# Kernel optimization log

Hardware: AMD Instinct MI355X
Metric: run time of the kernel (lower is better)

The kernel has to match this reference:

```python
import jax, jax.numpy as jnp
import numpy as np

DIM = 768
NUM_HEADS = 12
HEAD_DIM = DIM // NUM_HEADS
ALL_HEAD_DIM = HEAD_DIM * NUM_HEADS
SCALE = HEAD_DIM ** -0.5


def setup_inputs() -> dict:
    key = jax.random.key(0)
    k1, k2, k3, k4 = jax.random.split(key, 4)
    B, N = 8, 1024
    x = jax.random.normal(k1, (B, N, DIM), dtype=jnp.float32)
    # qkv_bias=False -> no qkv bias; proj has bias (nn.Linear default)
    w_qkv = jax.random.normal(k2, (DIM, 3 * ALL_HEAD_DIM), dtype=jnp.float32) * (DIM ** -0.5)
    w_proj = jax.random.normal(k3, (ALL_HEAD_DIM, DIM), dtype=jnp.float32) * (ALL_HEAD_DIM ** -0.5)
    b_proj = jax.random.normal(k4, (DIM,), dtype=jnp.float32) * 0.02
    return {"x": x, "w_qkv": w_qkv, "w_proj": w_proj, "b_proj": b_proj}


def reference(x, w_qkv, w_proj, b_proj):
    B, N, C = x.shape
    qkv = (x @ w_qkv).reshape(B, N, 3, NUM_HEADS, HEAD_DIM)
    qkv = jnp.transpose(qkv, (2, 0, 3, 1, 4))  # [3, B, H, N, D]
    q, k, v = qkv[0], qkv[1], qkv[2]
    attn = jax.nn.softmax(jnp.einsum('bhnd,bhmd->bhnm', q * SCALE, k), axis=-1)
    out = jnp.einsum('bhnm,bhmd->bhnd', attn, v)  # [B, H, N, D]
    out = jnp.transpose(out, (0, 2, 1, 3)).reshape(B, N, ALL_HEAD_DIM)
    return out @ w_proj + b_proj
```

## Files before the change

### kernel.cpp

```cpp
#include <hip/hip_runtime.h>
#include <hip/hip_bf16.h>

#define NH 12
#define HD 64
#define SEQ 1024
#define BATCH 8
#define DIM 768
#define QKVN 2304
#define ROWS 8192

typedef __bf16 bf16x8 __attribute__((ext_vector_type(8)));
typedef float f32x4 __attribute__((ext_vector_type(4)));
typedef unsigned short u16x8 __attribute__((ext_vector_type(8)));
typedef unsigned short u16x4 __attribute__((ext_vector_type(4)));
typedef short s16x4 __attribute__((ext_vector_type(4)));

__device__ __forceinline__ unsigned short f2bf(float f) {
  union { float f; unsigned int u; } c; c.f = f;
  unsigned int u = c.u;
  u += 0x7fffu + ((u >> 16) & 1u);
  return (unsigned short)(u >> 16);
}

__device__ __forceinline__ unsigned int pk_bf16(float a, float b) {
  union { __hip_bfloat162 h; unsigned int w; } u;
  u.h = __float22bfloat162_rn(float2{a, b});
  return u.w;
}

__device__ __forceinline__ void gload_lds16(const unsigned short* g, unsigned short* l) {
  __builtin_amdgcn_global_load_lds(
      (const __attribute__((address_space(1))) void*)g,
      (__attribute__((address_space(3))) void*)l, 16, 0, 0);
}

__device__ __forceinline__ void tr_tile(const float* __restrict__ src, unsigned short* __restrict__ dst,
                                        int R, int C, int bx, int by, float tile[32][33]) {
  int tx = threadIdx.x & 31, ty = threadIdx.x >> 5;
  int c0 = bx * 32, r0 = by * 32;
#pragma unroll
  for (int i = 0; i < 4; ++i)
    tile[ty + i * 8][tx] = src[(size_t)(r0 + ty + i * 8) * C + c0 + tx];
  __syncthreads();
#pragma unroll
  for (int i = 0; i < 4; ++i)
    dst[(size_t)(c0 + ty + i * 8) * R + r0 + tx] = f2bf(tile[tx][ty + i * 8]);
}

__global__ void prep_kernel(const float* __restrict__ x, unsigned short* __restrict__ xb,
                            const float* __restrict__ w_qkv, unsigned short* __restrict__ wqkvT,
                            const float* __restrict__ w_proj, unsigned short* __restrict__ wprojT) {
  __shared__ float tile[32][33];
  int blk = blockIdx.x;
  if (blk < 6144) {
    int i = blk * 256 + threadIdx.x;
    float4 v = ((const float4*)x)[i];
    unsigned int lo = pk_bf16(v.x, v.y), hi = pk_bf16(v.z, v.w);
    union { unsigned int w[2]; u16x4 o; } u; u.w[0] = lo; u.w[1] = hi;
    ((u16x4*)xb)[i] = u.o;
  } else if (blk < 6144 + 1728) {
    int t = blk - 6144;
    tr_tile(w_qkv, wqkvT, DIM, QKVN, t % 72, t / 72, tile);
  } else {
    int t = blk - 6144 - 1728;
    tr_tile(w_proj, wprojT, DIM, DIM, t % 24, t / 24, tile);
  }
}

template <bool BF16_OUT, bool SCALE_Q>
__global__ __launch_bounds__(256, 3) void gemm192(
    const unsigned short* __restrict__ A, const unsigned short* __restrict__ BT,
    void* __restrict__ Cout, const float* __restrict__ bias,
    int M, int N, int K, int nbyXCD) {
  __shared__ unsigned short As[2][128 * 32];
  __shared__ unsigned short Bs[2][192 * 32];
  const int tid = threadIdx.x;
  const int wave = tid >> 6, lane = tid & 63, quad = lane >> 4, l16 = lane & 15;
  const int wm = wave >> 1, wn = wave & 1;
  const int g = blockIdx.x & 7, bi = blockIdx.x >> 3;
  const int by = g * nbyXCD + (bi % nbyXCD);
  const int bx = bi / nbyXCD;
  const int bm = by * 128, bn = bx * 192;

  const int r0 = tid >> 2, kc0 = (tid & 3) * 8;
  const unsigned short* Ag = A + (size_t)(bm + r0) * K + kc0;
  const unsigned short* Bg = BT + (size_t)(bn + r0) * K + kc0;
  unsigned short* AsB = &As[0][0];
  unsigned short* BsB = &Bs[0][0];
  const int wdst = (tid & ~63) * 8;

#define STAGE_G(kt, b) do {                                                   \
    int koff_ = (kt) * 32;                                                    \
    gload_lds16(Ag + koff_,                    AsB + (b) * 4096 + wdst);      \
    gload_lds16(Ag + koff_ + (size_t)64 * K,   AsB + (b) * 4096 + wdst + 2048);\
    gload_lds16(Bg + koff_,                    BsB + (b) * 6144 + wdst);      \
    gload_lds16(Bg + koff_ + (size_t)64 * K,   BsB + (b) * 6144 + wdst + 2048);\
    gload_lds16(Bg + koff_ + (size_t)128 * K,  BsB + (b) * 6144 + wdst + 4096);\
  } while (0)

  f32x4 zero4 = {0.f, 0.f, 0.f, 0.f};
  f32x4 acc[4][6];
#pragma unroll
  for (int i = 0; i < 4; ++i)
#pragma unroll
    for (int j = 0; j < 6; ++j) acc[i][j] = zero4;

  const int nkt = K >> 5;
  STAGE_G(0, 0);
  for (int kt = 0; kt < nkt; ++kt) {
    __syncthreads();
    if (kt + 1 < nkt) STAGE_G(kt + 1, (kt + 1) & 1);
    const unsigned short* Ab = AsB + (kt & 1) * 4096;
    const unsigned short* Bb = BsB + (kt & 1) * 6144;
    bf16x8 af[4], bf[6];
#pragma unroll
    for (int mt = 0; mt < 4; ++mt)
      af[mt] = *(const bf16x8*)&Ab[(wm * 64 + mt * 16 + l16) * 32 + quad * 8];
#pragma unroll
    for (int nt = 0; nt < 6; ++nt)
      bf[nt] = *(const bf16x8*)&Bb[(wn * 96 + nt * 16 + l16) * 32 + quad * 8];
#pragma unroll
    for (int mt = 0; mt < 4; ++mt)
#pragma unroll
      for (int nt = 0; nt < 6; ++nt)
        acc[mt][nt] = __builtin_amdgcn_mfma_f32_16x16x32_bf16(af[mt], bf[nt], acc[mt][nt], 0, 0, 0);
  }
#undef STAGE_G

#pragma unroll
  for (int mt = 0; mt < 4; ++mt)
#pragma unroll
    for (int nt = 0; nt < 6; ++nt) {
      int col = bn + wn * 96 + nt * 16 + l16;
      float bv = BF16_OUT ? 0.f : bias[col];
      float scl = (SCALE_Q && col < DIM) ? 0.125f : 1.0f;
#pragma unroll
      for (int r = 0; r < 4; ++r) {
        int row = bm + wm * 64 + mt * 16 + quad * 4 + r;
        float v = acc[mt][nt][r];
        if (BF16_OUT)
          ((unsigned short*)Cout)[(size_t)row * N + col] = f2bf(v * scl);
        else
          ((float*)Cout)[(size_t)row * N + col] = v + bv;
      }
    }
}

__global__ __launch_bounds__(256, 5) void gemm64_proj(
    const unsigned short* __restrict__ A, const unsigned short* __restrict__ BT,
    float* __restrict__ Cout, const float* __restrict__ bias,
    int M, int N, int K, int nbyXCD) {
  __shared__ unsigned short As[2][128 * 32];
  __shared__ unsigned short Bs[2][64 * 32];
  const int tid = threadIdx.x;
  const int wave = tid >> 6, lane = tid & 63, quad = lane >> 4, l16 = lane & 15;
  const int g = blockIdx.x & 7, bi = blockIdx.x >> 3;
  const int by = g * nbyXCD + (bi % nbyXCD);
  const int bx = bi / nbyXCD;
  const int bm = by * 128, bn = bx * 64;

  const int r0 = tid >> 2, kc0 = (tid & 3) * 8;
  const unsigned short* Ag = A + (size_t)(bm + r0) * K + kc0;
  const unsigned short* Bg = BT + (size_t)(bn + r0) * K + kc0;
  unsigned short* AsB = &As[0][0];
  unsigned short* BsB = &Bs[0][0];
  const int wdst = (tid & ~63) * 8;

#define STAGE_P(kt, b) do {                                                    \
    int koff_ = (kt) * 32;                                                     \
    gload_lds16(Ag + koff_,                  AsB + (b) * 4096 + wdst);         \
    gload_lds16(Ag + koff_ + (size_t)64 * K, AsB + (b) * 4096 + wdst + 2048);  \
    gload_lds16(Bg + koff_,                  BsB + (b) * 2048 + wdst);         \
  } while (0)

  f32x4 zero4 = {0.f, 0.f, 0.f, 0.f};
  f32x4 acc[2][4];
#pragma unroll
  for (int i = 0; i < 2; ++i)
#pragma unroll
    for (int j = 0; j < 4; ++j) acc[i][j] = zero4;

  const int nkt = K >> 5;
  STAGE_P(0, 0);
  for (int kt = 0; kt < nkt; ++kt) {
    __syncthreads();
    if (kt + 1 < nkt) STAGE_P(kt + 1, (kt + 1) & 1);
    const unsigned short* Ab = AsB + (kt & 1) * 4096;
    const unsigned short* Bb = BsB + (kt & 1) * 2048;
    bf16x8 af[2], bf[4];
#pragma unroll
    for (int mt = 0; mt < 2; ++mt)
      af[mt] = *(const bf16x8*)&Ab[(wave * 32 + mt * 16 + l16) * 32 + quad * 8];
#pragma unroll
    for (int nt = 0; nt < 4; ++nt)
      bf[nt] = *(const bf16x8*)&Bb[(nt * 16 + l16) * 32 + quad * 8];
#pragma unroll
    for (int mt = 0; mt < 2; ++mt)
#pragma unroll
      for (int nt = 0; nt < 4; ++nt)
        acc[mt][nt] = __builtin_amdgcn_mfma_f32_16x16x32_bf16(af[mt], bf[nt], acc[mt][nt], 0, 0, 0);
  }
#undef STAGE_P

#pragma unroll
  for (int mt = 0; mt < 2; ++mt)
#pragma unroll
    for (int nt = 0; nt < 4; ++nt) {
      int col = bn + nt * 16 + l16;
      float bv = bias[col];
#pragma unroll
      for (int r = 0; r < 4; ++r) {
        int row = bm + wave * 32 + mt * 16 + quad * 4 + r;
        Cout[(size_t)row * N + col] = acc[mt][nt][r] + bv;
      }
    }
}

#define VS 76
__global__ __launch_bounds__(512, 6) void attn_kernel(
    const unsigned short* __restrict__ qkv, unsigned short* __restrict__ out) {
  __shared__ unsigned short Ks[2][64 * 64];
  __shared__ unsigned short Vts[2][64 * VS];

  const int tid = threadIdx.x;
  const int wave = tid >> 6, lane = tid & 63, quad = lane >> 4, l16 = lane & 15;
  const int x = blockIdx.x;
  const int qt = (x >> 3) & 7;
  const int bh = (x & 7) + 8 * (x >> 6);
  const int b = bh / NH, h = bh % NH;
  const int qcol = h * HD, kcol = DIM + h * HD, vcol = 2 * DIM + h * HD;
  const int rowQ0 = b * SEQ + qt * 128;
  const int rowKV0 = b * SEQ;

  const int kk_s = tid >> 8, rem_s = tid & 255, n_s = rem_s >> 2, kc_s = rem_s & 3;
  const unsigned short* kgp = qkv + (size_t)(rowKV0 + n_s) * QKVN + kcol + kk_s * 32 + kc_s * 8;
  unsigned short* klp = &Ks[0][0] + (tid & ~63) * 8;
  const int vn = tid & 63, vd0 = (tid >> 6) * 8;
  const unsigned short* vgp = qkv + (size_t)(rowKV0 + vn) * QKVN + vcol + vd0;

  bf16x8 qf[2];
  {
    const unsigned short* qp = qkv + (size_t)(rowQ0 + wave * 16 + l16) * QKVN + qcol + quad * 8;
    qf[0] = *(const bf16x8*)qp;
    qf[1] = *(const bf16x8*)(qp + 32);
  }

  gload_lds16(kgp, klp);
  {
    u16x8 v0 = *(const u16x8*)vgp;
    unsigned short* vb = &Vts[0][0];
#pragma unroll
    for (int e = 0; e < 8; ++e)
      vb[(vd0 + e) * VS + vn] = v0[e];
  }

  f32x4 zero4 = {0.f, 0.f, 0.f, 0.f};
  f32x4 o[4];
#pragma unroll
  for (int dt = 0; dt < 4; ++dt) o[dt] = zero4;
  float lsum = 0.f;

  for (int jt = 0; jt < 16; ++jt) {
    __syncthreads();
    u16x8 vnext;
    if (jt < 15) {
      gload_lds16(kgp + (size_t)(jt + 1) * 64 * QKVN, klp + ((jt + 1) & 1) * 4096);
      vnext = *(const u16x8*)(vgp + (size_t)(jt + 1) * 64 * QKVN);
    }

    const unsigned short* Kb = &Ks[jt & 1][0];
    const unsigned short* Vb = &Vts[jt & 1][0];

    f32x4 s[4];
#pragma unroll
    for (int nt = 0; nt < 4; ++nt) s[nt] = zero4;
#pragma unroll
    for (int kk = 0; kk < 2; ++kk)
#pragma unroll
      for (int nt = 0; nt < 4; ++nt) {
        bf16x8 kf = *(const bf16x8*)&Kb[kk * 2048 + (nt * 16 + l16) * 32 + quad * 8];
        s[nt] = __builtin_amdgcn_mfma_f32_16x16x32_bf16(kf, qf[kk], s[nt], 0, 0, 0);
      }

    s16x4 pf[4];
#pragma unroll
    for (int nt = 0; nt < 4; ++nt) {
      float p0 = __expf(s[nt][0]);
      float p1 = __expf(s[nt][1]);
      float p2 = __expf(s[nt][2]);
      float p3 = __expf(s[nt][3]);
      lsum += (p0 + p1) + (p2 + p3);
      union { unsigned int w[2]; s16x4 v; } u;
      u.w[0] = pk_bf16(p0, p1);
      u.w[1] = pk_bf16(p2, p3);
      pf[nt] = u.v;
    }

#pragma unroll
    for (int nt = 0; nt < 4; ++nt)
#pragma unroll
      for (int dt = 0; dt < 4; ++dt) {
        s16x4 vv = *(const s16x4*)&Vb[(dt * 16 + l16) * VS + nt * 16 + quad * 4];
        o[dt] = __builtin_amdgcn_mfma_f32_16x16x16bf16_1k(pf[nt], vv, o[dt], 0, 0, 0);
      }

    if (jt < 15) {
      unsigned short* vb = &Vts[(jt + 1) & 1][0];
#pragma unroll
      for (int e = 0; e < 8; ++e)
        vb[(vd0 + e) * VS + vn] = vnext[e];
    }
  }

  float l = lsum;
  l += __shfl_xor(l, 16);
  l += __shfl_xor(l, 32);
#pragma unroll
  for (int r = 0; r < 4; ++r) {
    float inv = 1.f / __shfl(l, quad * 4 + r);
    int row = rowQ0 + wave * 16 + quad * 4 + r;
#pragma unroll
    for (int dt = 0; dt < 4; ++dt)
      out[(size_t)row * DIM + h * HD + dt * 16 + l16] = f2bf(o[dt][r] * inv);
  }
}

extern "C" void kernel_launch(void* const* d_in, const int* in_sizes, int n_in,
                              void* d_out, int out_size, void* d_ws, size_t ws_size,
                              hipStream_t stream) {
  const float* x = (const float*)d_in[0];
  const float* w_qkv = (const float*)d_in[1];
  const float* w_proj = (const float*)d_in[2];
  const float* b_proj = (const float*)d_in[3];
  float* outp = (float*)d_out;

  unsigned short* xb = (unsigned short*)d_ws;
  unsigned short* wqkvT = xb + (size_t)ROWS * DIM;
  unsigned short* wprojT = wqkvT + (size_t)QKVN * DIM;
  unsigned short* qkvb = wprojT + (size_t)DIM * DIM;
  unsigned short* attnb = xb;

  prep_kernel<<<dim3(6144 + 1728 + 576), 256, 0, stream>>>(x, xb, w_qkv, wqkvT, w_proj, wprojT);
  gemm192<true, true><<<dim3(768), 256, 0, stream>>>(xb, wqkvT, qkvb, nullptr, ROWS, QKVN, DIM, 8);
  attn_kernel<<<dim3(8 * 96), 512, 0, stream>>>(qkvb, attnb);
  gemm64_proj<<<dim3(768), 256, 0, stream>>>(attnb, wprojT, outp, b_proj, ROWS, DIM, DIM, 8);
}
```

Before: 183.1 us.

## Process two query subtiles per wave in attention with 256-thread blocks

Halves the attention block to 4 waves, each computing 32 query rows as two 16-row subtiles. Every K and V fragment read from shared memory now feeds two MFMAs, and each thread issues two global loads per K/V stage. This targets LDS traffic and sync overhead per query row. The cost is doubled accumulator and score registers per wave and fewer waves per block to hide latency.

```diff
diff --git a/kernel.cpp b/kernel.cpp
--- a/kernel.cpp
+++ b/kernel.cpp
@@ -217,7 +217,7 @@
 }
 
 #define VS 76
-__global__ __launch_bounds__(512, 6) void attn_kernel(
+__global__ __launch_bounds__(256, 3) void attn_kernel(
     const unsigned short* __restrict__ qkv, unsigned short* __restrict__ out) {
   __shared__ unsigned short Ks[2][64 * 64];
   __shared__ unsigned short Vts[2][64 * VS];
@@ -232,96 +232,118 @@
   const int rowQ0 = b * SEQ + qt * 128;
   const int rowKV0 = b * SEQ;
 
-  const int kk_s = tid >> 8, rem_s = tid & 255, n_s = rem_s >> 2, kc_s = rem_s & 3;
-  const unsigned short* kgp = qkv + (size_t)(rowKV0 + n_s) * QKVN + kcol + kk_s * 32 + kc_s * 8;
+  const int n_s = tid >> 2, kc_s = tid & 3;
+  const unsigned short* kgp = qkv + (size_t)(rowKV0 + n_s) * QKVN + kcol + kc_s * 8;
   unsigned short* klp = &Ks[0][0] + (tid & ~63) * 8;
   const int vn = tid & 63, vd0 = (tid >> 6) * 8;
   const unsigned short* vgp = qkv + (size_t)(rowKV0 + vn) * QKVN + vcol + vd0;
 
-  bf16x8 qf[2];
+  bf16x8 qf[2][2];
+#pragma unroll
+  for (int sub = 0; sub < 2; ++sub) {
+    const unsigned short* qp = qkv + (size_t)(rowQ0 + wave * 32 + sub * 16 + l16) * QKVN + qcol + quad * 8;
+    qf[sub][0] = *(const bf16x8*)qp;
+    qf[sub][1] = *(const bf16x8*)(qp + 32);
+  }
+
+  gload_lds16(kgp, klp);
+  gload_lds16(kgp + 32, klp + 2048);
   {
-    const unsigned short* qp = qkv + (size_t)(rowQ0 + wave * 16 + l16) * QKVN + qcol + quad * 8;
-    qf[0] = *(const bf16x8*)qp;
-    qf[1] = *(const bf16x8*)(qp + 32);
-  }
-
-  gload_lds16(kgp, klp);
-  {
-    u16x8 v0 = *(const u16x8*)vgp;
+    u16x8 v0a = *(const u16x8*)vgp;
+    u16x8 v0b = *(const u16x8*)(vgp + 32);
     unsigned short* vb = &Vts[0][0];
 #pragma unroll
-    for (int e = 0; e < 8; ++e)
-      vb[(vd0 + e) * VS + vn] = v0[e];
+    for (int e = 0; e < 8; ++e) {
+      vb[(vd0 + e) * VS + vn] = v0a[e];
+      vb[(vd0 + 32 + e) * VS + vn] = v0b[e];
+    }
   }
 
   f32x4 zero4 = {0.f, 0.f, 0.f, 0.f};
-  f32x4 o[4];
-#pragma unroll
-  for (int dt = 0; dt < 4; ++dt) o[dt] = zero4;
-  float lsum = 0.f;
+  f32x4 o[2][4];
+#pragma unroll
+  for (int sub = 0; sub < 2; ++sub)
+#pragma unroll
+    for (int dt = 0; dt < 4; ++dt) o[sub][dt] = zero4;
+  float lsum[2] = {0.f, 0.f};
 
   for (int jt = 0; jt < 16; ++jt) {
     __syncthreads();
-    u16x8 vnext;
+    u16x8 vna, vnb;
     if (jt < 15) {
-      gload_lds16(kgp + (size_t)(jt + 1) * 64 * QKVN, klp + ((jt + 1) & 1) * 4096);
-      vnext = *(const u16x8*)(vgp + (size_t)(jt + 1) * 64 * QKVN);
+      const size_t goff = (size_t)(jt + 1) * 64 * QKVN;
+      unsigned short* kd = klp + ((jt + 1) & 1) * 4096;
+      gload_lds16(kgp + goff, kd);
+      gload_lds16(kgp + goff + 32, kd + 2048);
+      vna = *(const u16x8*)(vgp + goff);
+      vnb = *(const u16x8*)(vgp + goff + 32);
     }
 
     const unsigned short* Kb = &Ks[jt & 1][0];
     const unsigned short* Vb = &Vts[jt & 1][0];
 
-    f32x4 s[4];
-#pragma unroll
-    for (int nt = 0; nt < 4; ++nt) s[nt] = zero4;
+    f32x4 s[2][4];
+#pragma unroll
+    for (int sub = 0; sub < 2; ++sub)
+#pragma unroll
+      for (int nt = 0; nt < 4; ++nt) s[sub][nt] = zero4;
 #pragma unroll
     for (int kk = 0; kk < 2; ++kk)
 #pragma unroll
       for (int nt = 0; nt < 4; ++nt) {
         bf16x8 kf = *(const bf16x8*)&Kb[kk * 2048 + (nt * 16 + l16) * 32 + quad * 8];
-        s[nt] = __builtin_amdgcn_mfma_f32_16x16x32_bf16(kf, qf[kk], s[nt], 0, 0, 0);
-      }
-
-    s16x4 pf[4];
-#pragma unroll
-    for (int nt = 0; nt < 4; ++nt) {
-      float p0 = __expf(s[nt][0]);
-      float p1 = __expf(s[nt][1]);
-      float p2 = __expf(s[nt][2]);
-      float p3 = __expf(s[nt][3]);
-      lsum += (p0 + p1) + (p2 + p3);
-      union { unsigned int w[2]; s16x4 v; } u;
-      u.w[0] = pk_bf16(p0, p1);
-      u.w[1] = pk_bf16(p2, p3);
-      pf[nt] = u.v;
-    }
+        s[0][nt] = __builtin_amdgcn_mfma_f32_16x16x32_bf16(kf, qf[0][kk], s[0][nt], 0, 0, 0);
+        s[1][nt] = __builtin_amdgcn_mfma_f32_16x16x32_bf16(kf, qf[1][kk], s[1][nt], 0, 0, 0);
+      }
+
+    s16x4 pf[2][4];
+#pragma unroll
+    for (int sub = 0; sub < 2; ++sub)
+#pragma unroll
+      for (int nt = 0; nt < 4; ++nt) {
+        float p0 = __expf(s[sub][nt][0]);
+        float p1 = __expf(s[sub][nt][1]);
+        float p2 = __expf(s[sub][nt][2]);
+        float p3 = __expf(s[sub][nt][3]);
+        lsum[sub] += (p0 + p1) + (p2 + p3);
+        union { unsigned int w[2]; s16x4 v; } u;
+        u.w[0] = pk_bf16(p0, p1);
+        u.w[1] = pk_bf16(p2, p3);
+        pf[sub][nt] = u.v;
+      }
 
 #pragma unroll
     for (int nt = 0; nt < 4; ++nt)
 #pragma unroll
       for (int dt = 0; dt < 4; ++dt) {
         s16x4 vv = *(const s16x4*)&Vb[(dt * 16 + l16) * VS + nt * 16 + quad * 4];
-        o[dt] = __builtin_amdgcn_mfma_f32_16x16x16bf16_1k(pf[nt], vv, o[dt], 0, 0, 0);
+        o[0][dt] = __builtin_amdgcn_mfma_f32_16x16x16bf16_1k(pf[0][nt], vv, o[0][dt], 0, 0, 0);
+        o[1][dt] = __builtin_amdgcn_mfma_f32_16x16x16bf16_1k(pf[1][nt], vv, o[1][dt], 0, 0, 0);
       }
 
     if (jt < 15) {
       unsigned short* vb = &Vts[(jt + 1) & 1][0];
 #pragma unroll
-      for (int e = 0; e < 8; ++e)
-        vb[(vd0 + e) * VS + vn] = vnext[e];
-    }
-  }
-
-  float l = lsum;
-  l += __shfl_xor(l, 16);
-  l += __shfl_xor(l, 32);
-#pragma unroll
-  for (int r = 0; r < 4; ++r) {
-    float inv = 1.f / __shfl(l, quad * 4 + r);
-    int row = rowQ0 + wave * 16 + quad * 4 + r;
-#pragma unroll
-    for (int dt = 0; dt < 4; ++dt)
-      out[(size_t)row * DIM + h * HD + dt * 16 + l16] = f2bf(o[dt][r] * inv);
+      for (int e = 0; e < 8; ++e) {
+        vb[(vd0 + e) * VS + vn] = vna[e];
+        vb[(vd0 + 32 + e) * VS + vn] = vnb[e];
+      }
+    }
+  }
+
+#pragma unroll
+  for (int sub = 0; sub < 2; ++sub) {
+    float l = lsum[sub];
+    l += __shfl_xor(l, 16);
+    l += __shfl_xor(l, 32);
+#pragma unroll
+    for (int r = 0; r < 4; ++r) {
+      float inv = 1.f / __shfl(l, quad * 4 + r);
+      int row = rowQ0 + wave * 32 + sub * 16 + quad * 4 + r;
+#pragma unroll
+      for (int dt = 0; dt < 4; ++dt)
+        out[(size_t)row * DIM + h * HD + dt * 16 + l16] = f2bf(o[sub][dt][r] * inv);
+    }
   }
 }
 
@@ -342,6 +364,6 @@
 
   prep_kernel<<<dim3(6144 + 1728 + 576), 256, 0, stream>>>(x, xb, w_qkv, wqkvT, w_proj, wprojT);
   gemm192<true, true><<<dim3(768), 256, 0, stream>>>(xb, wqkvT, qkvb, nullptr, ROWS, QKVN, DIM, 8);
-  attn_kernel<<<dim3(8 * 96), 512, 0, stream>>>(qkvb, attnb);
+  attn_kernel<<<dim3(8 * 96), 256, 0, stream>>>(qkvb, attnb);
   gemm64_proj<<<dim3(768), 256, 0, stream>>>(attnb, wprojT, outp, b_proj, ROWS, DIM, DIM, 8);
 }
```

Measured after the change: 182.3 us. About the same (-0.4%).
